# Kernel tuning notes

Hardware: AMD Instinct MI355X
Metric: run time of the kernel (lower is better)

## Reference

```python
import jax, jax.numpy as jnp
import numpy as np

# hyperparams (from init_kwargs)
D = 16          # stride d
L_CMP = 32      # compression block length
L_SLC = 64      # selection block length
WINDOW = 128    # sliding-window half width
BLOCK_Q = 64    # query block for P_slc pooling
TOP_K = 2       # selected blocks per query
HIDDEN = 128


def extract_blocks(x, l, d):
    # x: [b, s, h, dim] -> [b, h, n_blocks, l, dim], strided overlapping blocks
    b, s, h, dim = x.shape
    n = (s - l) // d + 1
    idx = (np.arange(n) * d)[:, None] + np.arange(l)[None, :]  # [n, l] static
    blocks = x[:, idx]                                          # [b, n, l, h, dim]
    return jnp.transpose(blocks, (0, 3, 1, 2, 4))


def slc_map(n_cmp, n_slc, alpha, beta):
    # M[i, j] = #{(m, n) : 0<=m<alpha, 0<=n<beta, alpha*j - m - n == i}
    # so that P_slc = P_cmp @ M reproduces compute_p_slc's triple loop.
    M = np.zeros((n_cmp, n_slc), dtype=np.float32)
    for j in range(n_slc):
        for m in range(alpha):
            for nn in range(beta):
                i = alpha * j - m - nn
                if 0 <= i < n_cmp:
                    M[i, j] += 1.0
    return jnp.asarray(M)


def setup_inputs() -> dict:
    key = jax.random.key(0)
    ks = jax.random.split(key, 9)
    b, s, h, dim = 2, 1024, 8, HIDDEN
    return {
        'q': jax.random.normal(ks[0], (b, s, h, dim), jnp.float32),
        'k': jax.random.normal(ks[1], (b, s, h, dim), jnp.float32),
        'v': jax.random.normal(ks[2], (b, s, h, dim), jnp.float32),
        'w_cmp_k': jax.random.normal(ks[3], (L_CMP,), jnp.float32) * (L_CMP ** -0.5),
        'b_cmp_k': jax.random.normal(ks[4], (1,), jnp.float32) * 0.02,
        'w_cmp_v': jax.random.normal(ks[5], (L_CMP,), jnp.float32) * (L_CMP ** -0.5),
        'b_cmp_v': jax.random.normal(ks[6], (1,), jnp.float32) * 0.02,
        'w_gate': jax.random.normal(ks[7], (3, HIDDEN), jnp.float32) * (HIDDEN ** -0.5),
        'b_gate': jax.random.normal(ks[8], (3,), jnp.float32) * 0.02,
    }


def reference(q, k, v, w_cmp_k, b_cmp_k, w_cmp_v, b_cmp_v, w_gate, b_gate):
    scale = q.shape[-1] ** -0.5
    b, s, h, dim = q.shape

    # ---- branch 1: compressed attention ----
    Kb_cmp = extract_blocks(k, L_CMP, D)                    # [b,h,n_cmp,l_cmp,dim]
    Vb_cmp = extract_blocks(v, L_CMP, D)
    K_cmp = jnp.einsum('bhnld,l->bhnd', Kb_cmp, w_cmp_k) + b_cmp_k
    V_cmp = jnp.einsum('bhnld,l->bhnd', Vb_cmp, w_cmp_v) + b_cmp_v
    # NOTE: the source DIVIDES by softmax_scale here (faithful to original)
    attn_cmp = jnp.einsum('bshd,bhnd->bhsn', q, K_cmp) / scale
    P_cmp = jax.nn.softmax(attn_cmp, axis=-1)               # [b,h,s,n_cmp]
    out_cmp = jnp.einsum('bhsn,bhnd->bshd', P_cmp, V_cmp)

    # ---- branch 2: top-k block selection attention ----
    Kb_slc = extract_blocks(k, L_SLC, D)                    # [b,h,n_slc,l_slc,dim]
    Vb_slc = extract_blocks(v, L_SLC, D)
    n_cmp, n_slc = Kb_cmp.shape[2], Kb_slc.shape[2]
    M = slc_map(n_cmp, n_slc, L_SLC // D, L_CMP // D)
    P_slc = jnp.einsum('bhsn,nj->bhsj', P_cmp, M)           # compute_p_slc
    # pool scores within each query block (compute_blockq_p_slc)
    P_grp = P_slc.reshape(b, h, s // BLOCK_Q, BLOCK_Q, n_slc).sum(axis=3, keepdims=True)
    P_slc = jnp.broadcast_to(P_grp, (b, h, s // BLOCK_Q, BLOCK_Q, n_slc)).reshape(b, h, s, n_slc)
    # GQA pooling is a no-op here (q_heads == kv_heads)
    _, idx = jax.lax.top_k(P_slc, TOP_K)                    # [b,h,s,k]
    K_slc = jnp.take_along_axis(Kb_slc[:, :, None], idx[..., None, None], axis=3)
    V_slc = jnp.take_along_axis(Vb_slc[:, :, None], idx[..., None, None], axis=3)
    K_slc = K_slc.reshape(b, h, s, TOP_K * L_SLC, dim)      # [b,h,s,k*l,dim]
    V_slc = V_slc.reshape(b, h, s, TOP_K * L_SLC, dim)
    # flash_attn with q_len==1 per query token, non-causal, proper scale
    attn_slc = jnp.einsum('bshd,bhskd->bhsk', q, K_slc) * scale
    P_s = jax.nn.softmax(attn_slc, axis=-1)
    out_slc = jnp.einsum('bhsk,bhskd->bshd', P_s, V_slc)

    # ---- branch 3: sliding window attention (non-causal, window=(W,W)) ----
    scores = jnp.einsum('bshd,bthd->bhst', q, k) * scale
    ii = jnp.arange(s)[:, None]
    jj = jnp.arange(s)[None, :]
    win = (jj >= ii - WINDOW) & (jj <= ii + WINDOW)
    scores = jnp.where(win[None, None], scores, -jnp.inf)
    P_w = jax.nn.softmax(scores, axis=-1)
    out_win = jnp.einsum('bhst,bthd->bshd', P_w, v)

    # ---- gated combine ----
    gate = jax.nn.sigmoid(jnp.einsum('bshd,cd->bshc', q, w_gate) + b_gate)  # [b,s,h,3]
    out_stack = jnp.stack([out_cmp, out_slc, out_win], axis=2)              # [b,s,3,h,d]
    return jnp.einsum('bshc,bschd->bshd', gate, out_stack)
```

## Files before the change

### kernel.cpp

```cpp
#include <hip/hip_runtime.h>
#include <math.h>

#define B 2
#define S 1024
#define H 8
#define DIM 128
#define NCMP 63
#define NSLC 61
#define LCMP 32
#define QB 64
#define NQB (S/QB)
#define WIN 128
#define SCALE 0.08838834764831845f

__global__ __launch_bounds__(128) void cmp_kv_kernel(
    const float* __restrict__ k, const float* __restrict__ v,
    const float* __restrict__ wck, const float* __restrict__ bck,
    const float* __restrict__ wcv, const float* __restrict__ bcv,
    float* __restrict__ Kc, float* __restrict__ Vc)
{
  int d = threadIdx.x;
  int n = blockIdx.x;
  int h = blockIdx.y;
  int b = blockIdx.z;
  int s0 = n * 16;
  float sk = 0.f, sv = 0.f;
  #pragma unroll
  for (int l = 0; l < LCMP; ++l) {
    size_t gi = (((size_t)b*S + s0 + l)*H + h)*(size_t)DIM + d;
    sk += wck[l] * k[gi];
    sv += wcv[l] * v[gi];
  }
  size_t oi = (((size_t)(b*H + h)*NCMP + n)*(size_t)DIM) + d;
  Kc[oi] = sk + bck[0];
  Vc[oi] = sv + bcv[0];
}

__device__ __forceinline__ float wave_max(float x) {
  #pragma unroll
  for (int off = 32; off > 0; off >>= 1) x = fmaxf(x, __shfl_xor(x, off));
  return x;
}
__device__ __forceinline__ float wave_sum(float x) {
  #pragma unroll
  for (int off = 32; off > 0; off >>= 1) x += __shfl_xor(x, off);
  return x;
}

__device__ __forceinline__ void stage_kT_global(const float* __restrict__ kg, int b, int h,
                                                int row0, int tid, float (*kTl)[65]) {
  #pragma unroll
  for (int r = 0; r < 8; ++r) {
    int idx = (r << 10) + tid;
    int j = idx >> 7, d = idx & 127;
    int row = row0 + j;
    float val = 0.f;
    if (row >= 0 && row < S) val = kg[(((size_t)b*S + row)*H + h)*(size_t)DIM + d];
    kTl[d][j] = val;
  }
}
__device__ __forceinline__ void stage_v_global(const float* __restrict__ vg, int b, int h,
                                               int row0, int tid, float (*vl)[DIM]) {
  #pragma unroll
  for (int r = 0; r < 8; ++r) {
    int idx = (r << 10) + tid;
    int j = idx >> 7, d = idx & 127;
    int row = row0 + j;
    float val = 0.f;
    if (row >= 0 && row < S) val = vg[(((size_t)b*S + row)*H + h)*(size_t)DIM + d];
    vl[j][d] = val;
  }
}

__device__ __forceinline__ void qk_tile(const float (*qld)[DIM], const float (*kTl)[65],
                                        int q0, int lane, float sc[4]) {
  float a0 = 0.f, a1 = 0.f, a2 = 0.f, a3 = 0.f;
  #pragma unroll 8
  for (int d4 = 0; d4 < DIM; d4 += 4) {
    float4 qa = *(const float4*)&qld[q0+0][d4];
    float4 qb = *(const float4*)&qld[q0+1][d4];
    float4 qc = *(const float4*)&qld[q0+2][d4];
    float4 qd = *(const float4*)&qld[q0+3][d4];
    float k0 = kTl[d4+0][lane];
    float k1 = kTl[d4+1][lane];
    float k2 = kTl[d4+2][lane];
    float k3 = kTl[d4+3][lane];
    a0 += qa.x*k0 + qa.y*k1 + qa.z*k2 + qa.w*k3;
    a1 += qb.x*k0 + qb.y*k1 + qb.z*k2 + qb.w*k3;
    a2 += qc.x*k0 + qc.y*k1 + qc.z*k2 + qc.w*k3;
    a3 += qd.x*k0 + qd.y*k1 + qd.z*k2 + qd.w*k3;
  }
  sc[0]=a0; sc[1]=a1; sc[2]=a2; sc[3]=a3;
}

__global__ __launch_bounds__(1024) void nsa_mega(
    const float* __restrict__ qg, const float* __restrict__ kg, const float* __restrict__ vg,
    const float* __restrict__ Kc, const float* __restrict__ Vc,
    const float* __restrict__ wgate, const float* __restrict__ bgate,
    float* __restrict__ outg)
{
  __shared__ float q_lds[QB][DIM];
  __shared__ float kT[DIM][65];
  __shared__ float v_lds[64][DIM];
  __shared__ float p_lds[QB][128];
  __shared__ float S_col[64];
  __shared__ float gw[3][DIM];
  __shared__ int   sel[2];

  const int tid  = threadIdx.x;
  const int lane = tid & 63;
  const int wid  = tid >> 6;
  const int qb   = blockIdx.x;
  const int h    = blockIdx.y;
  const int b    = blockIdx.z;
  const int bh   = b*H + h;
  const int q0   = wid * 4;
  const int iq0  = qb*QB + q0;

  #pragma unroll
  for (int r = 0; r < 8; ++r) {
    int idx = (r << 10) + tid;
    int qq = idx >> 7, d = idx & 127;
    q_lds[qq][d] = qg[(((size_t)b*S + qb*QB + qq)*H + h)*(size_t)DIM + d];
  }
  if (tid < 384) gw[tid >> 7][tid & 127] = wgate[tid];

  const float* KcBH = Kc + (size_t)bh*NCMP*DIM;
  const float* VcBH = Vc + (size_t)bh*NCMP*DIM;
  #pragma unroll
  for (int r = 0; r < 8; ++r) {
    int idx = (r << 10) + tid;
    if (idx < NCMP*DIM) {
      int j = idx >> 7, d = idx & 127;
      kT[d][j]    = KcBH[idx];
      v_lds[j][d] = VcBH[idx];
    }
  }
  if (tid < DIM) { kT[tid][63] = 0.f; v_lds[63][tid] = 0.f; }
  __syncthreads();

  float accC0[4] = {0,0,0,0}, accC1[4] = {0,0,0,0};
  {
    float sc[4];
    qk_tile(q_lds, kT, q0, lane, sc);
    #pragma unroll
    for (int qq = 0; qq < 4; ++qq) {
      float sv = (lane < NCMP) ? (sc[qq] / SCALE) : -INFINITY;
      float m = wave_max(sv);
      float p = expf(sv - m);
      float l = wave_sum(p);
      p_lds[q0+qq][lane] = p / l;
    }
  }
  __syncthreads();

  {
    int d0 = lane * 2;
    #pragma unroll 4
    for (int j = 0; j < 64; ++j) {
      float2 vv = *(const float2*)&v_lds[j][d0];
      #pragma unroll
      for (int qq = 0; qq < 4; ++qq) {
        float pj = p_lds[q0+qq][j];
        accC0[qq] += pj * vv.x;
        accC1[qq] += pj * vv.y;
      }
    }
  }

  if (wid == 0) {
    float ssum = 0.f;
    if (lane < NCMP) {
      for (int qq2 = 0; qq2 < QB; ++qq2) ssum += p_lds[qq2][lane];
    }
    S_col[lane] = ssum;
    asm volatile("s_waitcnt lgkmcnt(0)" ::: "memory");
    float val = -INFINITY;
    if (lane < NSLC) {
      const float wts[5] = {1.f, 2.f, 2.f, 2.f, 1.f};
      float a = 0.f;
      #pragma unroll
      for (int o = 0; o < 5; ++o) {
        int i = 4*lane - o;
        if (i >= 0 && i < NCMP) a += wts[o] * S_col[i];
      }
      val = a;
    }
    float v1 = val; int i1 = lane;
    #pragma unroll
    for (int off = 32; off > 0; off >>= 1) {
      float ov = __shfl_xor(v1, off); int oi = __shfl_xor(i1, off);
      if (ov > v1 || (ov == v1 && oi < i1)) { v1 = ov; i1 = oi; }
    }
    int s0i = i1;
    float v2 = (lane == s0i) ? -INFINITY : val; int i2 = lane;
    #pragma unroll
    for (int off = 32; off > 0; off >>= 1) {
      float ov = __shfl_xor(v2, off); int oi = __shfl_xor(i2, off);
      if (ov > v2 || (ov == v2 && oi < i2)) { v2 = ov; i2 = oi; }
    }
    if (lane == 0) { sel[0] = s0i; sel[1] = i2; }
  }
  __syncthreads();

  float accS0[4] = {0,0,0,0}, accS1[4] = {0,0,0,0};
  {
    int rowA = sel[0] * 16;
    int rowB = sel[1] * 16;
    float scA[4], scB[4];

    stage_kT_global(kg, b, h, rowA, tid, kT);
    __syncthreads();
    qk_tile(q_lds, kT, q0, lane, scA);
    __syncthreads();
    stage_kT_global(kg, b, h, rowB, tid, kT);
    __syncthreads();
    qk_tile(q_lds, kT, q0, lane, scB);

    #pragma unroll
    for (int qq = 0; qq < 4; ++qq) {
      float aA = scA[qq] * SCALE;
      float aB = scB[qq] * SCALE;
      float m = wave_max(fmaxf(aA, aB));
      float pA = expf(aA - m);
      float pB = expf(aB - m);
      float l = wave_sum(pA + pB);
      p_lds[q0+qq][lane]      = pA / l;
      p_lds[q0+qq][64 + lane] = pB / l;
    }
    __syncthreads();

    stage_v_global(vg, b, h, rowA, tid, v_lds);
    __syncthreads();
    {
      int d0 = lane * 2;
      #pragma unroll 4
      for (int j = 0; j < 64; ++j) {
        float2 vv = *(const float2*)&v_lds[j][d0];
        #pragma unroll
        for (int qq = 0; qq < 4; ++qq) {
          float pj = p_lds[q0+qq][j];
          accS0[qq] += pj * vv.x;
          accS1[qq] += pj * vv.y;
        }
      }
    }
    __syncthreads();
    stage_v_global(vg, b, h, rowB, tid, v_lds);
    __syncthreads();
    {
      int d0 = lane * 2;
      #pragma unroll 4
      for (int j = 0; j < 64; ++j) {
        float2 vv = *(const float2*)&v_lds[j][d0];
        #pragma unroll
        for (int qq = 0; qq < 4; ++qq) {
          float pj = p_lds[q0+qq][64 + j];
          accS0[qq] += pj * vv.x;
          accS1[qq] += pj * vv.y;
        }
      }
    }
  }

  float accW0[4] = {0,0,0,0}, accW1[4] = {0,0,0,0};
  float mW[4] = {-INFINITY,-INFINITY,-INFINITY,-INFINITY};
  float lW[4] = {0,0,0,0};

  for (int t = 0; t < 6; ++t) {
    __syncthreads();
    int jt = qb*QB - WIN + t*64;
    stage_kT_global(kg, b, h, jt, tid, kT);
    stage_v_global(vg, b, h, jt, tid, v_lds);
    __syncthreads();

    float sc[4];
    qk_tile(q_lds, kT, q0, lane, sc);
    int jabs = jt + lane;
    bool gv = (jabs >= 0) && (jabs < S);
    float alpha[4];
    #pragma unroll
    for (int qq = 0; qq < 4; ++qq) {
      int ig = iq0 + qq;
      bool valid = gv && (jabs >= ig - WIN) && (jabs <= ig + WIN);
      float sv = valid ? (sc[qq] * SCALE) : -INFINITY;
      float tmax = wave_max(sv);
      float mnew = fmaxf(mW[qq], tmax);
      float pj;
      if (mnew == -INFINITY) {
        pj = 0.f; alpha[qq] = 1.f;
      } else {
        alpha[qq] = expf(mW[qq] - mnew);
        pj = expf(sv - mnew);
        lW[qq] = lW[qq] * alpha[qq] + wave_sum(pj);
        mW[qq] = mnew;
      }
      p_lds[q0+qq][lane] = pj;
    }
    __syncthreads();

    int d0 = lane * 2;
    #pragma unroll
    for (int qq = 0; qq < 4; ++qq) { accW0[qq] *= alpha[qq]; accW1[qq] *= alpha[qq]; }
    #pragma unroll 4
    for (int j = 0; j < 64; ++j) {
      float2 vv = *(const float2*)&v_lds[j][d0];
      #pragma unroll
      for (int qq = 0; qq < 4; ++qq) {
        float pj = p_lds[q0+qq][j];
        accW0[qq] += pj * vv.x;
        accW1[qq] += pj * vv.y;
      }
    }
  }
  #pragma unroll
  for (int qq = 0; qq < 4; ++qq) { accW0[qq] /= lW[qq]; accW1[qq] /= lW[qq]; }

  {
    int d0 = lane * 2;
    #pragma unroll
    for (int qq = 0; qq < 4; ++qq) {
      int qi = q0 + qq;
      float g[3];
      #pragma unroll
      for (int c = 0; c < 3; ++c) {
        float part = q_lds[qi][d0] * gw[c][d0] + q_lds[qi][d0+1] * gw[c][d0+1];
        part = wave_sum(part);
        g[c] = 1.f / (1.f + expf(-(part + bgate[c])));
      }
      float o0 = g[0]*accC0[qq] + g[1]*accS0[qq] + g[2]*accW0[qq];
      float o1 = g[0]*accC1[qq] + g[1]*accS1[qq] + g[2]*accW1[qq];
      size_t oi = (((size_t)b*S + iq0 + qq)*H + h)*(size_t)DIM + d0;
      *(float2*)&outg[oi] = make_float2(o0, o1);
    }
  }
}

extern "C" void kernel_launch(void* const* d_in, const int* in_sizes, int n_in,
                              void* d_out, int out_size, void* d_ws, size_t ws_size,
                              hipStream_t stream) {
  const float* q   = (const float*)d_in[0];
  const float* k   = (const float*)d_in[1];
  const float* v   = (const float*)d_in[2];
  const float* wck = (const float*)d_in[3];
  const float* bck = (const float*)d_in[4];
  const float* wcv = (const float*)d_in[5];
  const float* bcv = (const float*)d_in[6];
  const float* wg  = (const float*)d_in[7];
  const float* bg  = (const float*)d_in[8];
  float* out = (float*)d_out;

  float* Kc = (float*)d_ws;
  float* Vc = Kc + (size_t)B*H*NCMP*DIM;

  cmp_kv_kernel<<<dim3(NCMP, H, B), 128, 0, stream>>>(k, v, wck, bck, wcv, bcv, Kc, Vc);
  nsa_mega<<<dim3(NQB, H, B), 1024, 0, stream>>>(q, k, v, Kc, Vc, wg, bg, out);
}
```

Before: 250.7 us.

## Restructure NSA kernel: swizzled row-major K tiles, direct-global V reads, triple-buffered window

Rewrites the fused kernel so K tiles are staged row-major as swizzled float4 in a three-slot LDS ring. The next window tile is prefetched into registers while the current one is computed, and the V@P products read V straight from global memory instead of staging it in LDS. Softmax max subtraction and online rescaling are dropped for the selection and window branches, and exps are normalized once at the end using fast __expf. The compression kernel is vectorized to two channels per thread. This cuts barriers and LDS traffic, but risks overflow without max subtraction and adds uncoalesced global V reads per wave.

```diff
diff --git a/kernel.cpp b/kernel.cpp
--- a/kernel.cpp
+++ b/kernel.cpp
@@ -7,33 +7,38 @@
 #define DIM 128
 #define NCMP 63
 #define NSLC 61
-#define LCMP 32
 #define QB 64
 #define NQB (S/QB)
 #define WIN 128
-#define SCALE 0.08838834764831845f
-
-__global__ __launch_bounds__(128) void cmp_kv_kernel(
+#define SCALE  0.08838834764831845f
+#define RSCALE 11.313708498984761f
+
+typedef float v2f __attribute__((ext_vector_type(2)));
+
+__global__ __launch_bounds__(64) void cmp_kv_kernel(
     const float* __restrict__ k, const float* __restrict__ v,
     const float* __restrict__ wck, const float* __restrict__ bck,
     const float* __restrict__ wcv, const float* __restrict__ bcv,
     float* __restrict__ Kc, float* __restrict__ Vc)
 {
-  int d = threadIdx.x;
-  int n = blockIdx.x;
-  int h = blockIdx.y;
-  int b = blockIdx.z;
-  int s0 = n * 16;
-  float sk = 0.f, sv = 0.f;
-  #pragma unroll
-  for (int l = 0; l < LCMP; ++l) {
-    size_t gi = (((size_t)b*S + s0 + l)*H + h)*(size_t)DIM + d;
-    sk += wck[l] * k[gi];
-    sv += wcv[l] * v[gi];
-  }
-  size_t oi = (((size_t)(b*H + h)*NCMP + n)*(size_t)DIM) + d;
-  Kc[oi] = sk + bck[0];
-  Vc[oi] = sv + bcv[0];
+  const int d0 = threadIdx.x * 2;
+  const int n = blockIdx.x, h = blockIdx.y, b = blockIdx.z;
+  const size_t rs = (size_t)H * DIM;
+  const float* kp = k + (size_t)b*S*rs + (size_t)(n*16)*rs + (size_t)h*DIM + d0;
+  const float* vp = v + (kp - k);
+  v2f sk = {0.f, 0.f}, sv = {0.f, 0.f};
+  #pragma unroll
+  for (int l = 0; l < 32; ++l) {
+    v2f kk = *(const v2f*)(kp + (size_t)l*rs);
+    v2f vv = *(const v2f*)(vp + (size_t)l*rs);
+    sk += kk * wck[l];
+    sv += vv * wcv[l];
+  }
+  sk += bck[0];
+  sv += bcv[0];
+  size_t oi = ((size_t)(b*H + h)*NCMP + n)*(size_t)DIM + d0;
+  *(v2f*)(Kc + oi) = sk;
+  *(v2f*)(Vc + oi) = sv;
 }
 
 __device__ __forceinline__ float wave_max(float x) {
@@ -47,50 +52,47 @@
   return x;
 }
 
-__device__ __forceinline__ void stage_kT_global(const float* __restrict__ kg, int b, int h,
-                                                int row0, int tid, float (*kTl)[65]) {
-  #pragma unroll
-  for (int r = 0; r < 8; ++r) {
-    int idx = (r << 10) + tid;
-    int j = idx >> 7, d = idx & 127;
+__device__ __forceinline__ void qk4(const float (*q_lds)[DIM], const float4 (*k4)[32],
+                                    int q0, int lane, float sc[4]) {
+  v2f a0[4], a1[4];
+  #pragma unroll
+  for (int qq = 0; qq < 4; ++qq) { a0[qq] = (v2f){0.f,0.f}; a1[qq] = (v2f){0.f,0.f}; }
+  const int jsw = lane & 7;
+  #pragma unroll
+  for (int g = 0; g < 32; ++g) {
+    float4 kk = k4[lane][g ^ jsw];
+    v2f k01 = {kk.x, kk.y};
+    v2f k23 = {kk.z, kk.w};
+    #pragma unroll
+    for (int qq = 0; qq < 4; ++qq) {
+      float4 qv = *(const float4*)&q_lds[q0 + qq][g << 2];
+      v2f q01 = {qv.x, qv.y};
+      v2f q23 = {qv.z, qv.w};
+      a0[qq] += q01 * k01;
+      a1[qq] += q23 * k23;
+    }
+  }
+  #pragma unroll
+  for (int qq = 0; qq < 4; ++qq)
+    sc[qq] = (a0[qq].x + a0[qq].y) + (a1[qq].x + a1[qq].y);
+}
+
+__device__ __forceinline__ void pv_global(const float* __restrict__ vbase, size_t rowstride,
+                                          int row0, int rowmax,
+                                          const float (*p_lds)[64], int g0, int lane,
+                                          v2f acc[4]) {
+  const int d0 = lane * 2;
+  #pragma unroll 8
+  for (int j = 0; j < 64; ++j) {
+    float4 pv = *(const float4*)&p_lds[j][((g0 ^ (j & 15)) << 2)];
     int row = row0 + j;
-    float val = 0.f;
-    if (row >= 0 && row < S) val = kg[(((size_t)b*S + row)*H + h)*(size_t)DIM + d];
-    kTl[d][j] = val;
-  }
-}
-__device__ __forceinline__ void stage_v_global(const float* __restrict__ vg, int b, int h,
-                                               int row0, int tid, float (*vl)[DIM]) {
-  #pragma unroll
-  for (int r = 0; r < 8; ++r) {
-    int idx = (r << 10) + tid;
-    int j = idx >> 7, d = idx & 127;
-    int row = row0 + j;
-    float val = 0.f;
-    if (row >= 0 && row < S) val = vg[(((size_t)b*S + row)*H + h)*(size_t)DIM + d];
-    vl[j][d] = val;
-  }
-}
-
-__device__ __forceinline__ void qk_tile(const float (*qld)[DIM], const float (*kTl)[65],
-                                        int q0, int lane, float sc[4]) {
-  float a0 = 0.f, a1 = 0.f, a2 = 0.f, a3 = 0.f;
-  #pragma unroll 8
-  for (int d4 = 0; d4 < DIM; d4 += 4) {
-    float4 qa = *(const float4*)&qld[q0+0][d4];
-    float4 qb = *(const float4*)&qld[q0+1][d4];
-    float4 qc = *(const float4*)&qld[q0+2][d4];
-    float4 qd = *(const float4*)&qld[q0+3][d4];
-    float k0 = kTl[d4+0][lane];
-    float k1 = kTl[d4+1][lane];
-    float k2 = kTl[d4+2][lane];
-    float k3 = kTl[d4+3][lane];
-    a0 += qa.x*k0 + qa.y*k1 + qa.z*k2 + qa.w*k3;
-    a1 += qb.x*k0 + qb.y*k1 + qb.z*k2 + qb.w*k3;
-    a2 += qc.x*k0 + qc.y*k1 + qc.z*k2 + qc.w*k3;
-    a3 += qd.x*k0 + qd.y*k1 + qd.z*k2 + qd.w*k3;
-  }
-  sc[0]=a0; sc[1]=a1; sc[2]=a2; sc[3]=a3;
+    row = row < 0 ? 0 : (row > rowmax ? rowmax : row);
+    v2f vv = *(const v2f*)(vbase + (size_t)row*rowstride + d0);
+    acc[0] += vv * pv.x;
+    acc[1] += vv * pv.y;
+    acc[2] += vv * pv.z;
+    acc[3] += vv * pv.w;
+  }
 }
 
 __global__ __launch_bounds__(1024) void nsa_mega(
@@ -99,79 +101,84 @@
     const float* __restrict__ wgate, const float* __restrict__ bgate,
     float* __restrict__ outg)
 {
-  __shared__ float q_lds[QB][DIM];
-  __shared__ float kT[DIM][65];
-  __shared__ float v_lds[64][DIM];
-  __shared__ float p_lds[QB][128];
+  __shared__ __align__(16) float q_lds[QB][DIM];
+  __shared__ float4 kb[3][64][32];
+  __shared__ __align__(16) float p_lds[64][64];
   __shared__ float S_col[64];
-  __shared__ float gw[3][DIM];
+  __shared__ __align__(16) float gw[3][DIM];
   __shared__ int   sel[2];
 
   const int tid  = threadIdx.x;
   const int lane = tid & 63;
   const int wid  = tid >> 6;
-  const int qb   = blockIdx.x;
-  const int h    = blockIdx.y;
-  const int b    = blockIdx.z;
-  const int bh   = b*H + h;
-  const int q0   = wid * 4;
-  const int iq0  = qb*QB + q0;
-
-  #pragma unroll
-  for (int r = 0; r < 8; ++r) {
-    int idx = (r << 10) + tid;
-    int qq = idx >> 7, d = idx & 127;
-    q_lds[qq][d] = qg[(((size_t)b*S + qb*QB + qq)*H + h)*(size_t)DIM + d];
-  }
-  if (tid < 384) gw[tid >> 7][tid & 127] = wgate[tid];
-
-  const float* KcBH = Kc + (size_t)bh*NCMP*DIM;
-  const float* VcBH = Vc + (size_t)bh*NCMP*DIM;
-  #pragma unroll
-  for (int r = 0; r < 8; ++r) {
-    int idx = (r << 10) + tid;
-    if (idx < NCMP*DIM) {
-      int j = idx >> 7, d = idx & 127;
-      kT[d][j]    = KcBH[idx];
-      v_lds[j][d] = VcBH[idx];
-    }
-  }
-  if (tid < DIM) { kT[tid][63] = 0.f; v_lds[63][tid] = 0.f; }
-  __syncthreads();
-
-  float accC0[4] = {0,0,0,0}, accC1[4] = {0,0,0,0};
+  const int qb = blockIdx.x, h = blockIdx.y, b = blockIdx.z;
+  const int bh = b*H + h;
+  const int q0  = wid * 4;
+  const int iq0 = qb*QB + q0;
+  const size_t rs = (size_t)H * DIM;
+  const float* qg_bh = qg + (size_t)b*S*rs + (size_t)h*DIM;
+  const float* kg_bh = kg + (size_t)b*S*rs + (size_t)h*DIM;
+  const float* vg_bh = vg + (size_t)b*S*rs + (size_t)h*DIM;
+  const float* KcBH  = Kc + (size_t)bh*NCMP*DIM;
+  const float* VcBH  = Vc + (size_t)bh*NCMP*DIM;
+
+  const int ju0  = tid >> 5;
+  const int gu   = tid & 31;
+  const int jsw0 = ju0 & 7;
+
+  {
+    int qrow = qb*QB + ju0;
+    *(float4*)&q_lds[ju0][gu*4]    = *(const float4*)(qg_bh + (size_t)qrow*rs + gu*4);
+    *(float4*)&q_lds[ju0+32][gu*4] = *(const float4*)(qg_bh + (size_t)(qrow+32)*rs + gu*4);
+    if (tid < 384) gw[tid >> 7][tid & 127] = wgate[tid];
+
+    float4 c0 = *(const float4*)(KcBH + (size_t)ju0*DIM + gu*4);
+    float4 c1 = (ju0+32 < NCMP) ? *(const float4*)(KcBH + (size_t)(ju0+32)*DIM + gu*4)
+                                : make_float4(0.f,0.f,0.f,0.f);
+    kb[2][ju0][gu ^ jsw0]    = c0;
+    kb[2][ju0+32][gu ^ jsw0] = c1;
+
+    int row0 = qb*QB - WIN;
+    int r = row0 + ju0;
+    float4 w0 = (r >= 0 && r < S) ? *(const float4*)(kg_bh + (size_t)r*rs + gu*4)
+                                  : make_float4(0.f,0.f,0.f,0.f);
+    r = row0 + ju0 + 32;
+    float4 w1 = (r >= 0 && r < S) ? *(const float4*)(kg_bh + (size_t)r*rs + gu*4)
+                                  : make_float4(0.f,0.f,0.f,0.f);
+    kb[0][ju0][gu ^ jsw0]    = w0;
+    kb[0][ju0+32][gu ^ jsw0] = w1;
+  }
+  __syncthreads();
+
+  const int pcolg = ((wid ^ (lane & 15)) << 2);
+
+  v2f accC[4];
+  #pragma unroll
+  for (int qq = 0; qq < 4; ++qq) accC[qq] = (v2f){0.f,0.f};
   {
     float sc[4];
-    qk_tile(q_lds, kT, q0, lane, sc);
-    #pragma unroll
-    for (int qq = 0; qq < 4; ++qq) {
-      float sv = (lane < NCMP) ? (sc[qq] / SCALE) : -INFINITY;
-      float m = wave_max(sv);
-      float p = expf(sv - m);
+    qk4(q_lds, kb[2], q0, lane, sc);
+    float4 p4;
+    #pragma unroll
+    for (int qq = 0; qq < 4; ++qq) {
+      float svv = (lane < NCMP) ? sc[qq]*RSCALE : -INFINITY;
+      float m = wave_max(svv);
+      float p = __expf(svv - m);
       float l = wave_sum(p);
-      p_lds[q0+qq][lane] = p / l;
-    }
-  }
-  __syncthreads();
-
-  {
-    int d0 = lane * 2;
-    #pragma unroll 4
-    for (int j = 0; j < 64; ++j) {
-      float2 vv = *(const float2*)&v_lds[j][d0];
-      #pragma unroll
-      for (int qq = 0; qq < 4; ++qq) {
-        float pj = p_lds[q0+qq][j];
-        accC0[qq] += pj * vv.x;
-        accC1[qq] += pj * vv.y;
-      }
-    }
-  }
+      ((float*)&p4)[qq] = p * (1.f/l);
+    }
+    *(float4*)&p_lds[lane][pcolg] = p4;
+    pv_global(VcBH, DIM, 0, NCMP-1, p_lds, wid, lane, accC);
+  }
+  __syncthreads();
 
   if (wid == 0) {
     float ssum = 0.f;
-    if (lane < NCMP) {
-      for (int qq2 = 0; qq2 < QB; ++qq2) ssum += p_lds[qq2][lane];
+    const int gx = lane & 15;
+    #pragma unroll
+    for (int g = 0; g < 16; ++g) {
+      float4 t4 = *(const float4*)&p_lds[lane][(g ^ gx) << 2];
+      ssum += (t4.x + t4.y) + (t4.z + t4.w);
     }
     S_col[lane] = ssum;
     asm volatile("s_waitcnt lgkmcnt(0)" ::: "memory");
@@ -203,136 +210,117 @@
   }
   __syncthreads();
 
-  float accS0[4] = {0,0,0,0}, accS1[4] = {0,0,0,0};
-  {
-    int rowA = sel[0] * 16;
-    int rowB = sel[1] * 16;
+  const int rowA = sel[0] * 16;
+  const int rowB = sel[1] * 16;
+  {
+    float4 a0 = *(const float4*)(kg_bh + (size_t)(rowA+ju0)*rs + gu*4);
+    float4 a1 = *(const float4*)(kg_bh + (size_t)(rowA+ju0+32)*rs + gu*4);
+    kb[1][ju0][gu ^ jsw0]    = a0;
+    kb[1][ju0+32][gu ^ jsw0] = a1;
+    float4 b0_ = *(const float4*)(kg_bh + (size_t)(rowB+ju0)*rs + gu*4);
+    float4 b1_ = *(const float4*)(kg_bh + (size_t)(rowB+ju0+32)*rs + gu*4);
+    kb[2][ju0][gu ^ jsw0]    = b0_;
+    kb[2][ju0+32][gu ^ jsw0] = b1_;
+  }
+  float4 wA, wB;
+  {
+    int row0 = qb*QB - WIN + 64;
+    int r = row0 + ju0;
+    wA = (r >= 0 && r < S) ? *(const float4*)(kg_bh + (size_t)r*rs + gu*4)
+                           : make_float4(0.f,0.f,0.f,0.f);
+    r = row0 + ju0 + 32;
+    wB = (r >= 0 && r < S) ? *(const float4*)(kg_bh + (size_t)r*rs + gu*4)
+                           : make_float4(0.f,0.f,0.f,0.f);
+  }
+  __syncthreads();
+
+  v2f accS[4];
+  float lsumS[4] = {0.f,0.f,0.f,0.f};
+  #pragma unroll
+  for (int qq = 0; qq < 4; ++qq) accS[qq] = (v2f){0.f,0.f};
+  {
     float scA[4], scB[4];
-
-    stage_kT_global(kg, b, h, rowA, tid, kT);
-    __syncthreads();
-    qk_tile(q_lds, kT, q0, lane, scA);
-    __syncthreads();
-    stage_kT_global(kg, b, h, rowB, tid, kT);
-    __syncthreads();
-    qk_tile(q_lds, kT, q0, lane, scB);
-
-    #pragma unroll
-    for (int qq = 0; qq < 4; ++qq) {
-      float aA = scA[qq] * SCALE;
-      float aB = scB[qq] * SCALE;
-      float m = wave_max(fmaxf(aA, aB));
-      float pA = expf(aA - m);
-      float pB = expf(aB - m);
-      float l = wave_sum(pA + pB);
-      p_lds[q0+qq][lane]      = pA / l;
-      p_lds[q0+qq][64 + lane] = pB / l;
-    }
-    __syncthreads();
-
-    stage_v_global(vg, b, h, rowA, tid, v_lds);
-    __syncthreads();
-    {
-      int d0 = lane * 2;
-      #pragma unroll 4
-      for (int j = 0; j < 64; ++j) {
-        float2 vv = *(const float2*)&v_lds[j][d0];
-        #pragma unroll
-        for (int qq = 0; qq < 4; ++qq) {
-          float pj = p_lds[q0+qq][j];
-          accS0[qq] += pj * vv.x;
-          accS1[qq] += pj * vv.y;
-        }
-      }
-    }
-    __syncthreads();
-    stage_v_global(vg, b, h, rowB, tid, v_lds);
-    __syncthreads();
-    {
-      int d0 = lane * 2;
-      #pragma unroll 4
-      for (int j = 0; j < 64; ++j) {
-        float2 vv = *(const float2*)&v_lds[j][d0];
-        #pragma unroll
-        for (int qq = 0; qq < 4; ++qq) {
-          float pj = p_lds[q0+qq][64 + j];
-          accS0[qq] += pj * vv.x;
-          accS1[qq] += pj * vv.y;
-        }
-      }
-    }
-  }
-
-  float accW0[4] = {0,0,0,0}, accW1[4] = {0,0,0,0};
-  float mW[4] = {-INFINITY,-INFINITY,-INFINITY,-INFINITY};
-  float lW[4] = {0,0,0,0};
+    qk4(q_lds, kb[1], q0, lane, scA);
+    qk4(q_lds, kb[2], q0, lane, scB);
+    float4 p4;
+    #pragma unroll
+    for (int qq = 0; qq < 4; ++qq) {
+      float pA = __expf(scA[qq]*SCALE);
+      ((float*)&p4)[qq] = pA;
+      lsumS[qq] += pA;
+    }
+    *(float4*)&p_lds[lane][pcolg] = p4;
+    pv_global(vg_bh, rs, rowA, S-1, p_lds, wid, lane, accS);
+    #pragma unroll
+    for (int qq = 0; qq < 4; ++qq) {
+      float pB = __expf(scB[qq]*SCALE);
+      ((float*)&p4)[qq] = pB;
+      lsumS[qq] += pB;
+    }
+    *(float4*)&p_lds[lane][pcolg] = p4;
+    pv_global(vg_bh, rs, rowB, S-1, p_lds, wid, lane, accS);
+  }
+  __syncthreads();
+
+  v2f accW[4];
+  float lsumW[4] = {0.f,0.f,0.f,0.f};
+  #pragma unroll
+  for (int qq = 0; qq < 4; ++qq) accW[qq] = (v2f){0.f,0.f};
 
   for (int t = 0; t < 6; ++t) {
-    __syncthreads();
-    int jt = qb*QB - WIN + t*64;
-    stage_kT_global(kg, b, h, jt, tid, kT);
-    stage_v_global(vg, b, h, jt, tid, v_lds);
-    __syncthreads();
-
+    int row0 = qb*QB - WIN + t*64;
+    if (t < 5) {
+      int nb = (t+1) % 3;
+      kb[nb][ju0][gu ^ jsw0]    = wA;
+      kb[nb][ju0+32][gu ^ jsw0] = wB;
+    }
+    if (t < 4) {
+      int r0n = qb*QB - WIN + (t+2)*64;
+      int r = r0n + ju0;
+      wA = (r >= 0 && r < S) ? *(const float4*)(kg_bh + (size_t)r*rs + gu*4)
+                             : make_float4(0.f,0.f,0.f,0.f);
+      r = r0n + ju0 + 32;
+      wB = (r >= 0 && r < S) ? *(const float4*)(kg_bh + (size_t)r*rs + gu*4)
+                             : make_float4(0.f,0.f,0.f,0.f);
+    }
     float sc[4];
-    qk_tile(q_lds, kT, q0, lane, sc);
-    int jabs = jt + lane;
-    bool gv = (jabs >= 0) && (jabs < S);
-    float alpha[4];
+    qk4(q_lds, kb[t % 3], q0, lane, sc);
+    int jabs = row0 + lane;
+    bool jin = (jabs >= 0) & (jabs < S);
+    float4 p4;
     #pragma unroll
     for (int qq = 0; qq < 4; ++qq) {
       int ig = iq0 + qq;
-      bool valid = gv && (jabs >= ig - WIN) && (jabs <= ig + WIN);
-      float sv = valid ? (sc[qq] * SCALE) : -INFINITY;
-      float tmax = wave_max(sv);
-      float mnew = fmaxf(mW[qq], tmax);
-      float pj;
-      if (mnew == -INFINITY) {
-        pj = 0.f; alpha[qq] = 1.f;
-      } else {
-        alpha[qq] = expf(mW[qq] - mnew);
-        pj = expf(sv - mnew);
-        lW[qq] = lW[qq] * alpha[qq] + wave_sum(pj);
-        mW[qq] = mnew;
-      }
-      p_lds[q0+qq][lane] = pj;
-    }
-    __syncthreads();
-
-    int d0 = lane * 2;
-    #pragma unroll
-    for (int qq = 0; qq < 4; ++qq) { accW0[qq] *= alpha[qq]; accW1[qq] *= alpha[qq]; }
-    #pragma unroll 4
-    for (int j = 0; j < 64; ++j) {
-      float2 vv = *(const float2*)&v_lds[j][d0];
-      #pragma unroll
-      for (int qq = 0; qq < 4; ++qq) {
-        float pj = p_lds[q0+qq][j];
-        accW0[qq] += pj * vv.x;
-        accW1[qq] += pj * vv.y;
-      }
-    }
-  }
-  #pragma unroll
-  for (int qq = 0; qq < 4; ++qq) { accW0[qq] /= lW[qq]; accW1[qq] /= lW[qq]; }
-
-  {
-    int d0 = lane * 2;
-    #pragma unroll
-    for (int qq = 0; qq < 4; ++qq) {
-      int qi = q0 + qq;
-      float g[3];
-      #pragma unroll
-      for (int c = 0; c < 3; ++c) {
-        float part = q_lds[qi][d0] * gw[c][d0] + q_lds[qi][d0+1] * gw[c][d0+1];
-        part = wave_sum(part);
-        g[c] = 1.f / (1.f + expf(-(part + bgate[c])));
-      }
-      float o0 = g[0]*accC0[qq] + g[1]*accS0[qq] + g[2]*accW0[qq];
-      float o1 = g[0]*accC1[qq] + g[1]*accS1[qq] + g[2]*accW1[qq];
-      size_t oi = (((size_t)b*S + iq0 + qq)*H + h)*(size_t)DIM + d0;
-      *(float2*)&outg[oi] = make_float2(o0, o1);
-    }
+      bool valid = jin & (jabs >= ig - WIN) & (jabs <= ig + WIN);
+      float pj = valid ? __expf(sc[qq]*SCALE) : 0.f;
+      ((float*)&p4)[qq] = pj;
+      lsumW[qq] += pj;
+    }
+    *(float4*)&p_lds[lane][pcolg] = p4;
+    pv_global(vg_bh, rs, row0, S-1, p_lds, wid, lane, accW);
+    if (t < 5) __syncthreads();
+  }
+
+  float lS[4], lW[4];
+  #pragma unroll
+  for (int qq = 0; qq < 4; ++qq) { lS[qq] = wave_sum(lsumS[qq]); lW[qq] = wave_sum(lsumW[qq]); }
+
+  const int d0 = lane * 2;
+  #pragma unroll
+  for (int qq = 0; qq < 4; ++qq) {
+    int qi = q0 + qq;
+    v2f qv = *(const v2f*)&q_lds[qi][d0];
+    float g_[3];
+    #pragma unroll
+    for (int c = 0; c < 3; ++c) {
+      v2f gwv = *(const v2f*)&gw[c][d0];
+      float part = qv.x*gwv.x + qv.y*gwv.y;
+      part = wave_sum(part);
+      g_[c] = 1.f / (1.f + __expf(-(part + bgate[c])));
+    }
+    v2f o = accC[qq]*g_[0] + accS[qq]*(g_[1]/lS[qq]) + accW[qq]*(g_[2]/lW[qq]);
+    size_t oi = (size_t)b*S*rs + (size_t)(iq0+qq)*rs + (size_t)h*DIM + d0;
+    *(v2f*)(outg + oi) = o;
   }
 }
 
@@ -353,6 +341,6 @@
   float* Kc = (float*)d_ws;
   float* Vc = Kc + (size_t)B*H*NCMP*DIM;
 
-  cmp_kv_kernel<<<dim3(NCMP, H, B), 128, 0, stream>>>(k, v, wck, bck, wcv, bcv, Kc, Vc);
+  cmp_kv_kernel<<<dim3(NCMP, H, B), 64, 0, stream>>>(k, v, wck, bck, wcv, bcv, Kc, Vc);
   nsa_mega<<<dim3(NQB, H, B), 1024, 0, stream>>>(q, k, v, Kc, Vc, wg, bg, out);
 }
```

Result: slower. 776.1 us (+209.6%).
